# Kernel optimization log

Hardware: AMD Instinct MI355X
Metric: run time of the kernel (lower is better)

## Reference

```python
import jax, jax.numpy as jnp
import numpy as np

D_MODEL = 1024
N_HEADS = 16
HEAD_DIM = D_MODEL // N_HEADS
B, S = 4, 2048
NEG = -1000000000.0


def setup_inputs() -> dict:
    key = jax.random.key(0)
    ks = jax.random.split(key, 13)
    sc = 1.0 / np.sqrt(D_MODEL)
    return {
        "query": jax.random.normal(ks[0], (B, S, D_MODEL), jnp.float32),
        "key": jax.random.normal(ks[1], (B, S, D_MODEL), jnp.float32),
        "value": jax.random.normal(ks[2], (B, S, D_MODEL), jnp.float32),
        "mask": jax.random.randint(ks[3], (B, 1, 1, S), 0, 2, jnp.int32),
        "Wq": jax.random.normal(ks[4], (D_MODEL, D_MODEL), jnp.float32) * sc,
        "bq": jax.random.normal(ks[5], (D_MODEL,), jnp.float32) * sc,
        "Wk": jax.random.normal(ks[6], (D_MODEL, D_MODEL), jnp.float32) * sc,
        "bk": jax.random.normal(ks[7], (D_MODEL,), jnp.float32) * sc,
        "Wv": jax.random.normal(ks[8], (D_MODEL, D_MODEL), jnp.float32) * sc,
        "bv": jax.random.normal(ks[9], (D_MODEL,), jnp.float32) * sc,
        "Wo": jax.random.normal(ks[10], (D_MODEL, D_MODEL), jnp.float32) * sc,
        "bo": jax.random.normal(ks[11], (D_MODEL,), jnp.float32) * sc,
    }


def _split_heads(x):
    b, s, _ = x.shape
    return x.reshape(b, s, N_HEADS, HEAD_DIM).transpose(0, 2, 1, 3)  # (B,H,S,Dh)


def reference(query, key, value, mask, Wq, bq, Wk, bk, Wv, bv, Wo, bo):
    # torch Linear: y = x @ W.T + b
    Q = _split_heads(query @ Wq.T + bq)
    K = _split_heads(key @ Wk.T + bk)
    V = _split_heads(value @ Wv.T + bv)
    scores = jnp.einsum("bhqd,bhkd->bhqk", Q, K) / np.sqrt(HEAD_DIM)
    scores = jnp.where(mask == 0, NEG, scores)
    probs = jax.nn.softmax(scores, axis=-1)
    ctx = jnp.einsum("bhqk,bhkd->bhqd", probs, V)
    ctx = ctx.transpose(0, 2, 1, 3).reshape(query.shape[0], query.shape[1], D_MODEL)
    return ctx @ Wo.T + bo
```

## Files before the change

kernel.cpp:

```cpp
#include <hip/hip_runtime.h>


typedef __bf16 bf16x8 __attribute__((ext_vector_type(8)));
typedef __bf16 bf16x4 __attribute__((ext_vector_type(4)));
typedef float  f32x4  __attribute__((ext_vector_type(4)));

#define LOG2E 1.44269504088896340736f
#define SCALE_Q (0.125f * LOG2E)
#define MBIAS_L2 (-1.44269504e9f)
#define MFMA16(a, b, c) __builtin_amdgcn_mfma_f32_16x16x32_bf16(a, b, c, 0, 0, 0)

__device__ inline unsigned short f2bf(float f) {
  unsigned int u = __float_as_uint(f);
  u = u + 0x7FFF + ((u >> 16) & 1);
  return (unsigned short)(u >> 16);
}
__device__ inline void gload16(const void* g, void* l) {
  __builtin_amdgcn_global_load_lds(
      (const __attribute__((address_space(1))) void*)g,
      (__attribute__((address_space(3))) void*)l, 16, 0, 0);
}
__device__ inline bf16x8 cvt8(const float* p) {
  float4 a = *(const float4*)p, b = *(const float4*)(p + 4);
  bf16x8 v;
  v[0] = (__bf16)a.x; v[1] = (__bf16)a.y; v[2] = (__bf16)a.z; v[3] = (__bf16)a.w;
  v[4] = (__bf16)b.x; v[5] = (__bf16)b.y; v[6] = (__bf16)b.z; v[7] = (__bf16)b.w;
  return v;
}

struct CvtJob { const float* s; unsigned short* d; int n8; };
struct CvtJobs { CvtJob j[8]; };
__global__ void cvt_all(CvtJobs J) {
  CvtJob jb = J.j[blockIdx.y];
  int i = blockIdx.x * 256 + threadIdx.x;
  if (blockIdx.y == 7) {
    if (i < jb.n8) {
      int4 m = ((const int4*)jb.s)[i];
      float4 o;
      o.x = m.x ? 0.f : MBIAS_L2;
      o.y = m.y ? 0.f : MBIAS_L2;
      o.z = m.z ? 0.f : MBIAS_L2;
      o.w = m.w ? 0.f : MBIAS_L2;
      ((float4*)jb.d)[i] = o;
    }
    return;
  }
  if (i < jb.n8) *(bf16x8*)(jb.d + (size_t)i * 8) = cvt8(jb.s + (size_t)i * 8);
}

struct ProjJob { const unsigned short* A; const unsigned short* W;
                 const float* bias; unsigned short* out; float scale; };
struct ProjJobs { ProjJob j[3]; };

__global__ __launch_bounds__(256, 3) void gemm_qkv(ProjJobs J) {
  __shared__ __align__(16) unsigned short Al[2][128 * 32];
  __shared__ __align__(16) unsigned short Wl[2][128 * 32];
  const int z = blockIdx.z;
  const ProjJob jb = J.j[z];
  const int tid = threadIdx.x, lane = tid & 63, w = tid >> 6;
  const int lid = lane & 15, lg = lane >> 4;
  const int lin = blockIdx.x + 8 * (int)blockIdx.y;
  const int xcd = lin & 7, j = lin >> 3;
  const int c0 = (j & 7) * 128;
  const int t0 = ((j >> 3) * 8 + xcd) * 128;
  const int wm = (w & 1) * 64, wn = (w >> 1) * 64;

  f32x4 acc[4][4];
#pragma unroll
  for (int i = 0; i < 4; i++)
#pragma unroll
    for (int jj = 0; jj < 4; jj++) acc[i][jj] = (f32x4){0.f, 0.f, 0.f, 0.f};

  auto stage = [&](int bi, int kt) {
#pragma unroll
    for (int i = 0; i < 2; i++) {
      int c = i * 256 + tid, r = c >> 2, ko = (c & 3) * 8;
      gload16(jb.A + (size_t)(t0 + r) * 1024 + kt + ko, &Al[bi][c * 8]);
      gload16(jb.W + (size_t)(c0 + r) * 1024 + kt + ko, &Wl[bi][c * 8]);
    }
  };
  auto compute = [&](int bi) {
    const unsigned short* Ml = (z == 2) ? Al[bi] : Wl[bi];
    const unsigned short* Nl = (z == 2) ? Wl[bi] : Al[bi];
    bf16x8 mf[4], nf[4];
#pragma unroll
    for (int mi = 0; mi < 4; mi++)
      mf[mi] = *(const bf16x8*)(&Ml[(wm + mi * 16 + lid) * 32 + lg * 8]);
#pragma unroll
    for (int ni = 0; ni < 4; ni++)
      nf[ni] = *(const bf16x8*)(&Nl[(wn + ni * 16 + lid) * 32 + lg * 8]);
#pragma unroll
    for (int mi = 0; mi < 4; mi++)
#pragma unroll
      for (int ni = 0; ni < 4; ni++)
        acc[mi][ni] = MFMA16(mf[mi], nf[ni], acc[mi][ni]);
  };

  stage(0, 0);
  __syncthreads();
  for (int kt = 0; kt < 1024; kt += 64) {
    stage(1, kt + 32);
    compute(0);
    __syncthreads();
    if (kt + 64 < 1024) stage(0, kt + 64);
    compute(1);
    __syncthreads();
  }

  if (z < 2) {
    const float scale = jb.scale;
#pragma unroll
    for (int mi = 0; mi < 4; mi++) {
      int colb = c0 + wm + mi * 16 + lg * 4;
      float4 b4 = *(const float4*)(&jb.bias[colb]);
#pragma unroll
      for (int ni = 0; ni < 4; ni++) {
        int token = t0 + wn + ni * 16 + lid;
        ushort4 st;
        st.x = f2bf((acc[mi][ni][0] + b4.x) * scale);
        st.y = f2bf((acc[mi][ni][1] + b4.y) * scale);
        st.z = f2bf((acc[mi][ni][2] + b4.z) * scale);
        st.w = f2bf((acc[mi][ni][3] + b4.w) * scale);
        *(ushort4*)(&jb.out[(size_t)token * 1024 + colb]) = st;
      }
    }
  } else {
    const int b = t0 >> 11;
#pragma unroll
    for (int ni = 0; ni < 4; ni++) {
      int col = c0 + wn + ni * 16 + lid;
      int h = col >> 6, d = col & 63;
      float bv = jb.bias[col];
#pragma unroll
      for (int mi = 0; mi < 4; mi++) {
        int s = (t0 & 2047) + wm + mi * 16 + lg * 4;
        int sp = (s & ~31) | (((s >> 2) & 3) << 3) | (((s >> 4) & 1) << 2);
        ushort4 st;
        st.x = f2bf(acc[mi][ni][0] + bv);
        st.y = f2bf(acc[mi][ni][1] + bv);
        st.z = f2bf(acc[mi][ni][2] + bv);
        st.w = f2bf(acc[mi][ni][3] + bv);
        *(ushort4*)(&jb.out[(size_t)((b * 16 + h) * 64 + d) * 2048 + sp]) = st;
      }
    }
  }
}

__global__ __launch_bounds__(256, 4) void gemm_o(
    const unsigned short* __restrict__ A, const unsigned short* __restrict__ W,
    const float* __restrict__ bias, float* __restrict__ C) {
  __shared__ __align__(16) unsigned short Al[2][64 * 32];
  __shared__ __align__(16) unsigned short Wl[2][128 * 32];
  const int tid = threadIdx.x, lane = tid & 63, w = tid >> 6;
  const int lid = lane & 15, lg = lane >> 4;
  const int lin = blockIdx.x + 8 * (int)blockIdx.y;
  const int xcd = lin & 7, j = lin >> 3;
  const int c0 = (j & 7) * 128;
  const int t0 = ((j >> 3) * 8 + xcd) * 64;
  const int wc = (w & 1) * 64, wt = (w >> 1) * 32;
  f32x4 acc[4][2];
#pragma unroll
  for (int i = 0; i < 4; i++)
#pragma unroll
    for (int jj = 0; jj < 2; jj++) acc[i][jj] = (f32x4){0.f, 0.f, 0.f, 0.f};

  auto stage = [&](int bi, int kt) {
#pragma unroll
    for (int i = 0; i < 2; i++) {
      int c = i * 256 + tid, r = c >> 2, ko = (c & 3) * 8;
      gload16(W + (size_t)(c0 + r) * 1024 + kt + ko, &Wl[bi][c * 8]);
    }
    {
      int c = tid, r = c >> 2, ko = (c & 3) * 8;
      gload16(A + (size_t)(t0 + r) * 1024 + kt + ko, &Al[bi][c * 8]);
    }
  };
  auto compute = [&](int bi) {
    bf16x8 aw[4], bt[2];
#pragma unroll
    for (int mi = 0; mi < 4; mi++)
      aw[mi] = *(const bf16x8*)(&Wl[bi][(wc + mi * 16 + lid) * 32 + lg * 8]);
#pragma unroll
    for (int ni = 0; ni < 2; ni++)
      bt[ni] = *(const bf16x8*)(&Al[bi][(wt + ni * 16 + lid) * 32 + lg * 8]);
#pragma unroll
    for (int mi = 0; mi < 4; mi++)
#pragma unroll
      for (int ni = 0; ni < 2; ni++)
        acc[mi][ni] = MFMA16(aw[mi], bt[ni], acc[mi][ni]);
  };

  stage(0, 0);
  __syncthreads();
  for (int kt = 0; kt < 1024; kt += 64) {
    stage(1, kt + 32);
    compute(0);
    __syncthreads();
    if (kt + 64 < 1024) stage(0, kt + 64);
    compute(1);
    __syncthreads();
  }
#pragma unroll
  for (int mi = 0; mi < 4; mi++) {
    int colb = c0 + wc + mi * 16 + lg * 4;
    float4 b4 = *(const float4*)(&bias[colb]);
#pragma unroll
    for (int ni = 0; ni < 2; ni++) {
      int token = t0 + wt + ni * 16 + lid;
      float4 st;
      st.x = acc[mi][ni][0] + b4.x;
      st.y = acc[mi][ni][1] + b4.y;
      st.z = acc[mi][ni][2] + b4.z;
      st.w = acc[mi][ni][3] + b4.w;
      *(float4*)(&C[(size_t)token * 1024 + colb]) = st;
    }
  }
}

__global__ __launch_bounds__(256, 4) void attn(
    const unsigned short* __restrict__ Qp,
    const unsigned short* __restrict__ Kp,
    const unsigned short* __restrict__ Vt,
    const float* __restrict__ mbias,
    unsigned short* __restrict__ ctx) {
  __shared__ __align__(16) unsigned short Klds[2][64 * 64];
  __shared__ __align__(16) unsigned short Vlds[2][64 * 64];

  const int tid = threadIdx.x, lane = tid & 63, w = tid >> 6;
  const int lid = lane & 15, lg = lane >> 4;
  const int wg = blockIdx.x + (int)(gridDim.x) * blockIdx.y;
  const int xcd = wg & 7, idx = wg >> 3;
  const int bh = (xcd << 3) | (idx >> 4);
  const int q0 = (idx & 15) * 128;
  const int b = bh >> 4, h = bh & 15;
  const int wq = w * 32;
  const int x7 = lid & 7;

  const unsigned short* Kg = Kp + (size_t)(b * 2048) * 1024 + h * 64;
  const unsigned short* Vg = Vt + (size_t)bh * 64 * 2048;
  const float* mg = mbias + b * 2048;

  bf16x8 qf[2][2];
#pragma unroll
  for (int qt = 0; qt < 2; qt++)
#pragma unroll
    for (int ks = 0; ks < 2; ks++) {
      int qrow = b * 2048 + q0 + wq + qt * 16 + lid;
      qf[qt][ks] = *(const bf16x8*)(Qp + (size_t)qrow * 1024 + h * 64 + ks * 32 + lg * 8);
    }

  f32x4 Ot[4][2];
#pragma unroll
  for (int dt = 0; dt < 4; dt++)
#pragma unroll
    for (int qt = 0; qt < 2; qt++) Ot[dt][qt] = (f32x4){0.f, 0.f, 0.f, 0.f};
  f32x4 acc_l[2] = {(f32x4){0.f, 0.f, 0.f, 0.f}, (f32x4){0.f, 0.f, 0.f, 0.f}};
  bf16x8 ones8;
#pragma unroll
  for (int i = 0; i < 8; i++) ones8[i] = (__bf16)1.0f;

  auto stage_kv = [&](unsigned short* Kl, unsigned short* Vl, int k0) {
#pragma unroll
    for (int i = 0; i < 2; i++) {
      int c = i * 256 + tid, r = c >> 3, gsw = (c & 7) ^ (r & 7);
      gload16(Kg + (size_t)(k0 + r) * 1024 + gsw * 8, Kl + c * 8);
    }
#pragma unroll
    for (int i = 0; i < 2; i++) {
      int c = i * 256 + tid, d = c >> 3, gsw = (c & 7) ^ (d & 7);
      gload16(Vg + (size_t)d * 2048 + k0 + gsw * 8, Vl + c * 8);
    }
  };

  auto compute_tile = [&](const unsigned short* Kl, const unsigned short* Vl, int kt) {
    const float* mrow = mg + kt * 64;
    f32x4 accS[4][2];
#pragma unroll
    for (int mt = 0; mt < 4; mt++) {
      f32x4 mb4 = *(const f32x4*)(&mrow[mt * 16 + lg * 4]);
      accS[mt][0] = mb4;
      accS[mt][1] = mb4;
    }
    __builtin_amdgcn_s_setprio(1);
#pragma unroll
    for (int ks = 0; ks < 2; ks++) {
      int koff = ((ks * 4 + lg) ^ x7) * 8;
#pragma unroll
      for (int mt = 0; mt < 4; mt++) {
        bf16x8 a = *(const bf16x8*)(&Kl[(mt * 16 + lid) * 64 + koff]);
        accS[mt][0] = MFMA16(a, qf[0][ks], accS[mt][0]);
        accS[mt][1] = MFMA16(a, qf[1][ks], accS[mt][1]);
      }
    }
    __builtin_amdgcn_s_setprio(0);

    bf16x8 pb[2][2];
#pragma unroll
    for (int qt = 0; qt < 2; qt++)
#pragma unroll
      for (int mt = 0; mt < 4; mt++) {
        int half = (mt & 1) * 4;
#pragma unroll
        for (int r = 0; r < 4; r++) {
          float p = __builtin_amdgcn_exp2f(accS[mt][qt][r]);
          pb[mt >> 1][qt][half + r] = (__bf16)p;
        }
      }

    __builtin_amdgcn_s_setprio(1);
#pragma unroll
    for (int c = 0; c < 2; c++)
#pragma unroll
      for (int qt = 0; qt < 2; qt++)
        acc_l[qt] = MFMA16(ones8, pb[c][qt], acc_l[qt]);

#pragma unroll
    for (int c = 0; c < 2; c++) {
      int goff = (((c * 4 + lg) ^ x7)) * 8;
#pragma unroll
      for (int dt = 0; dt < 4; dt++) {
        bf16x8 av = *(const bf16x8*)(&Vl[(dt * 16 + lid) * 64 + goff]);
        Ot[dt][0] = MFMA16(av, pb[c][0], Ot[dt][0]);
        Ot[dt][1] = MFMA16(av, pb[c][1], Ot[dt][1]);
      }
    }
    __builtin_amdgcn_s_setprio(0);
  };

  stage_kv(&Klds[0][0], &Vlds[0][0], 0);
  __syncthreads();

  for (int kt = 0; kt < 32; kt += 2) {
    stage_kv(&Klds[1][0], &Vlds[1][0], (kt + 1) * 64);
    compute_tile(&Klds[0][0], &Vlds[0][0], kt);
    __syncthreads();
    if (kt + 2 < 32) stage_kv(&Klds[0][0], &Vlds[0][0], (kt + 2) * 64);
    compute_tile(&Klds[1][0], &Vlds[1][0], kt + 1);
    __syncthreads();
  }

#pragma unroll
  for (int qt = 0; qt < 2; qt++) {
    float inv = 1.0f / acc_l[qt][0];
    int qrow = b * 2048 + q0 + wq + qt * 16 + lid;
#pragma unroll
    for (int dt = 0; dt < 4; dt++) {
      ushort4 st;
      st.x = f2bf(Ot[dt][qt][0] * inv);
      st.y = f2bf(Ot[dt][qt][1] * inv);
      st.z = f2bf(Ot[dt][qt][2] * inv);
      st.w = f2bf(Ot[dt][qt][3] * inv);
      *(ushort4*)(&ctx[(size_t)qrow * 1024 + h * 64 + dt * 16 + lg * 4]) = st;
    }
  }
}

extern "C" void kernel_launch(void* const* d_in, const int* in_sizes, int n_in,
                              void* d_out, int out_size, void* d_ws, size_t ws_size,
                              hipStream_t stream) {
  const float* q  = (const float*)d_in[0];
  const float* k  = (const float*)d_in[1];
  const float* v  = (const float*)d_in[2];
  const int*   mk = (const int*)d_in[3];
  const float* Wq = (const float*)d_in[4];
  const float* bq = (const float*)d_in[5];
  const float* Wk = (const float*)d_in[6];
  const float* bk = (const float*)d_in[7];
  const float* Wv = (const float*)d_in[8];
  const float* bv = (const float*)d_in[9];
  const float* Wo = (const float*)d_in[10];
  const float* bo = (const float*)d_in[11];

  const size_t NTOK = (size_t)8192 * 1024;
  const size_t NW = (size_t)1024 * 1024;

  unsigned short* qb  = (unsigned short*)d_ws;
  unsigned short* kb  = qb + NTOK;
  unsigned short* vb  = kb + NTOK;
  unsigned short* Qp  = vb + NTOK;
  unsigned short* Kp  = Qp + NTOK;
  unsigned short* Vt  = Kp + NTOK;
  unsigned short* Wqb = Vt + NTOK;
  unsigned short* Wkb = Wqb + NW;
  unsigned short* Wvb = Wkb + NW;
  unsigned short* Wob = Wvb + NW;
  float*          mbg = (float*)(Wob + NW);
  unsigned short* ctx = qb;

  CvtJobs J;
  J.j[0] = {q, qb, (int)(NTOK / 8)};
  J.j[1] = {k, kb, (int)(NTOK / 8)};
  J.j[2] = {v, vb, (int)(NTOK / 8)};
  J.j[3] = {Wq, Wqb, (int)(NW / 8)};
  J.j[4] = {Wk, Wkb, (int)(NW / 8)};
  J.j[5] = {Wv, Wvb, (int)(NW / 8)};
  J.j[6] = {Wo, Wob, (int)(NW / 8)};
  J.j[7] = {(const float*)mk, (unsigned short*)mbg, 2048};
  cvt_all<<<dim3(4096, 8), 256, 0, stream>>>(J);

  ProjJobs P;
  P.j[0] = {qb, Wqb, bq, Qp, SCALE_Q};
  P.j[1] = {kb, Wkb, bk, Kp, 1.0f};
  P.j[2] = {vb, Wvb, bv, Vt, 1.0f};
  gemm_qkv<<<dim3(8, 64, 3), 256, 0, stream>>>(P);

  attn<<<dim3(16, 64), 256, 0, stream>>>(Qp, Kp, Vt, mbg, ctx);
  gemm_o<<<dim3(8, 128), 256, 0, stream>>>(ctx, Wob, bo, (float*)d_out);
}
```

Before: 333.8 us.

## Fuse fp32-to-bf16 activation conversion into QKV projection GEMM loads

Removes the separate conversion pass over the q/k/v activations. The QKV GEMM now reads fp32 activations directly into registers, converts them to bf16 and writes them to LDS, which saves writing and re-reading three bf16 copies. The cost is more register pressure and twice the global bytes per A tile, since fp32 is re-read by each of the 8 column blocks. The A loads also become synchronous register round-trips instead of async global-to-LDS loads.

```diff
diff --git a/kernel.cpp b/kernel.cpp
--- a/kernel.cpp
+++ b/kernel.cpp
@@ -27,13 +27,19 @@
   v[4] = (__bf16)b.x; v[5] = (__bf16)b.y; v[6] = (__bf16)b.z; v[7] = (__bf16)b.w;
   return v;
 }
+__device__ inline bf16x8 cvt8r(const float4& a, const float4& b) {
+  bf16x8 v;
+  v[0] = (__bf16)a.x; v[1] = (__bf16)a.y; v[2] = (__bf16)a.z; v[3] = (__bf16)a.w;
+  v[4] = (__bf16)b.x; v[5] = (__bf16)b.y; v[6] = (__bf16)b.z; v[7] = (__bf16)b.w;
+  return v;
+}
 
 struct CvtJob { const float* s; unsigned short* d; int n8; };
-struct CvtJobs { CvtJob j[8]; };
+struct CvtJobs { CvtJob j[5]; };
 __global__ void cvt_all(CvtJobs J) {
   CvtJob jb = J.j[blockIdx.y];
   int i = blockIdx.x * 256 + threadIdx.x;
-  if (blockIdx.y == 7) {
+  if (blockIdx.y == 4) {
     if (i < jb.n8) {
       int4 m = ((const int4*)jb.s)[i];
       float4 o;
@@ -48,7 +54,7 @@
   if (i < jb.n8) *(bf16x8*)(jb.d + (size_t)i * 8) = cvt8(jb.s + (size_t)i * 8);
 }
 
-struct ProjJob { const unsigned short* A; const unsigned short* W;
+struct ProjJob { const float* A; const unsigned short* W;
                  const float* bias; unsigned short* out; float scale; };
 struct ProjJobs { ProjJob j[3]; };
 
@@ -71,11 +77,26 @@
 #pragma unroll
     for (int jj = 0; jj < 4; jj++) acc[i][jj] = (f32x4){0.f, 0.f, 0.f, 0.f};
 
-  auto stage = [&](int bi, int kt) {
+  auto stage_load = [&](int kt, float4 (&ar)[2][2]) {
 #pragma unroll
     for (int i = 0; i < 2; i++) {
       int c = i * 256 + tid, r = c >> 2, ko = (c & 3) * 8;
-      gload16(jb.A + (size_t)(t0 + r) * 1024 + kt + ko, &Al[bi][c * 8]);
+      const float* ap = jb.A + (size_t)(t0 + r) * 1024 + kt + ko;
+      ar[i][0] = *(const float4*)ap;
+      ar[i][1] = *(const float4*)(ap + 4);
+    }
+  };
+  auto stage_write = [&](int bi, float4 (&ar)[2][2]) {
+#pragma unroll
+    for (int i = 0; i < 2; i++) {
+      int c = i * 256 + tid;
+      *(bf16x8*)(&Al[bi][c * 8]) = cvt8r(ar[i][0], ar[i][1]);
+    }
+  };
+  auto stage_W = [&](int bi, int kt) {
+#pragma unroll
+    for (int i = 0; i < 2; i++) {
+      int c = i * 256 + tid, r = c >> 2, ko = (c & 3) * 8;
       gload16(jb.W + (size_t)(c0 + r) * 1024 + kt + ko, &Wl[bi][c * 8]);
     }
   };
@@ -96,14 +117,24 @@
         acc[mi][ni] = MFMA16(mf[mi], nf[ni], acc[mi][ni]);
   };
 
-  stage(0, 0);
+  float4 arA[2][2], arB[2][2];
+  stage_load(0, arA);
+  stage_W(0, 0);
+  stage_write(0, arA);
   __syncthreads();
+
   for (int kt = 0; kt < 1024; kt += 64) {
-    stage(1, kt + 32);
+    stage_load(kt + 32, arB);
+    stage_W(1, kt + 32);
     compute(0);
-    __syncthreads();
-    if (kt + 64 < 1024) stage(0, kt + 64);
+    stage_write(1, arB);
+    __syncthreads();
+    if (kt + 64 < 1024) {
+      stage_load(kt + 64, arA);
+      stage_W(0, kt + 64);
+    }
     compute(1);
+    if (kt + 64 < 1024) stage_write(0, arA);
     __syncthreads();
   }
 
@@ -374,10 +405,8 @@
   const size_t NTOK = (size_t)8192 * 1024;
   const size_t NW = (size_t)1024 * 1024;
 
-  unsigned short* qb  = (unsigned short*)d_ws;
-  unsigned short* kb  = qb + NTOK;
-  unsigned short* vb  = kb + NTOK;
-  unsigned short* Qp  = vb + NTOK;
+  unsigned short* ctx = (unsigned short*)d_ws;
+  unsigned short* Qp  = ctx + NTOK;
   unsigned short* Kp  = Qp + NTOK;
   unsigned short* Vt  = Kp + NTOK;
   unsigned short* Wqb = Vt + NTOK;
@@ -385,23 +414,19 @@
   unsigned short* Wvb = Wkb + NW;
   unsigned short* Wob = Wvb + NW;
   float*          mbg = (float*)(Wob + NW);
-  unsigned short* ctx = qb;
 
   CvtJobs J;
-  J.j[0] = {q, qb, (int)(NTOK / 8)};
-  J.j[1] = {k, kb, (int)(NTOK / 8)};
-  J.j[2] = {v, vb, (int)(NTOK / 8)};
-  J.j[3] = {Wq, Wqb, (int)(NW / 8)};
-  J.j[4] = {Wk, Wkb, (int)(NW / 8)};
-  J.j[5] = {Wv, Wvb, (int)(NW / 8)};
-  J.j[6] = {Wo, Wob, (int)(NW / 8)};
-  J.j[7] = {(const float*)mk, (unsigned short*)mbg, 2048};
-  cvt_all<<<dim3(4096, 8), 256, 0, stream>>>(J);
+  J.j[0] = {Wq, Wqb, (int)(NW / 8)};
+  J.j[1] = {Wk, Wkb, (int)(NW / 8)};
+  J.j[2] = {Wv, Wvb, (int)(NW / 8)};
+  J.j[3] = {Wo, Wob, (int)(NW / 8)};
+  J.j[4] = {(const float*)mk, (unsigned short*)mbg, 2048};
+  cvt_all<<<dim3(512, 5), 256, 0, stream>>>(J);
 
   ProjJobs P;
-  P.j[0] = {qb, Wqb, bq, Qp, SCALE_Q};
-  P.j[1] = {kb, Wkb, bk, Kp, 1.0f};
-  P.j[2] = {vb, Wvb, bv, Vt, 1.0f};
+  P.j[0] = {q, Wqb, bq, Qp, SCALE_Q};
+  P.j[1] = {k, Wkb, bk, Kp, 1.0f};
+  P.j[2] = {v, Wvb, bv, Vt, 1.0f};
   gemm_qkv<<<dim3(8, 64, 3), 256, 0, stream>>>(P);
 
   attn<<<dim3(16, 64), 256, 0, stream>>>(Qp, Kp, Vt, mbg, ctx);
```

New measurement: 358.5 us. 1.07x slower.
